# Kernel tuning notes

Measured on AMD Instinct MI355X. Metric: run time of the kernel, lower is better.

The kernel has to match this reference:

```python
import jax, jax.numpy as jnp
import numpy as np

VOCAB = 401
E = 256   # embed_size
H = 768   # hidden_size
O = 3     # output_size
B = 64
T = 1024


def setup_inputs() -> dict:
    key = jax.random.key(0)
    ks = jax.random.split(key, 8)
    s = lambda fan_in: 1.0 / np.sqrt(fan_in)
    return {
        "tokens": jax.random.randint(ks[0], (B, T), 0, VOCAB),
        "hidden": jnp.zeros((B, H), dtype=jnp.float32),
        "embed": jax.random.normal(ks[1], (VOCAB, E), dtype=jnp.float32),
        "W_ih": jax.random.uniform(ks[2], (3 * H, E), jnp.float32, -s(H), s(H)),
        "W_hh": jax.random.uniform(ks[3], (3 * H, H), jnp.float32, -s(H), s(H)),
        "b_ih": jax.random.uniform(ks[4], (3 * H,), jnp.float32, -s(H), s(H)),
        "b_hh": jax.random.uniform(ks[5], (3 * H,), jnp.float32, -s(H), s(H)),
        "W_out": jax.random.uniform(ks[6], (O, H), jnp.float32, -s(H), s(H)),
        "b_out": jax.random.uniform(ks[7], (O,), jnp.float32, -s(H), s(H)),
    }


def reference(tokens, hidden, embed, W_ih, W_hh, b_ih, b_hh, W_out, b_out):
    # Embedding lookup for all timesteps: [B, T, E]
    x = embed[tokens]
    # Precompute input-to-hidden projections for all steps: [B, T, 3H]
    xi = jnp.einsum("bte,ge->btg", x, W_ih) + b_ih
    # Note: original forward zeroes the passed-in hidden; we honor that.
    h0 = jnp.zeros_like(hidden)

    def step(h, xt):  # xt: [B, 3H]
        gh = h @ W_hh.T + b_hh                      # [B, 3H]
        xr, xz, xn = jnp.split(xt, 3, axis=1)
        hr, hz, hn = jnp.split(gh, 3, axis=1)
        r = jax.nn.sigmoid(xr + hr)
        z = jax.nn.sigmoid(xz + hz)
        n = jnp.tanh(xn + r * hn)
        h_new = (1.0 - z) * n + z * h
        return h_new, None

    h_final, _ = jax.lax.scan(step, h0, jnp.swapaxes(xi, 0, 1))  # scan over T
    logits = h_final @ W_out.T + b_out                            # [B, O]
    logprobs = jax.nn.log_softmax(logits, axis=1)
    return (logprobs, h_final)
```

## Files before the change

### kernel.cpp

```cpp
#include <hip/hip_runtime.h>

#define VOCABN 401
#define EN 256
#define HN 768
#define H3N 2304
#define ON 3
#define BN 64
#define TN 1024

#define NREP 16
#define WGPR 16
#define BPR  4
#define JPW  48
#define NTH  768

typedef _Float16 f16x2 __attribute__((ext_vector_type(2)));
typedef _Float16 f16x8 __attribute__((ext_vector_type(8)));
typedef unsigned long long u64;
union F16x8 { f16x8 v; f16x2 p[4]; };

__device__ __forceinline__ float fdot2(f16x2 a, f16x2 b, float c) {
#if __has_builtin(__builtin_amdgcn_fdot2)
    return __builtin_amdgcn_fdot2(a, b, c, false);
#else
    return c + (float)a[0] * (float)b[0] + (float)a[1] * (float)b[1];
#endif
}

__device__ __forceinline__ float hexsum(float x) {
    int v = __builtin_bit_cast(int, x);
    x += __builtin_bit_cast(float, __builtin_amdgcn_update_dpp(0, v, 0xB1, 0xF, 0xF, true));
    v = __builtin_bit_cast(int, x);
    x += __builtin_bit_cast(float, __builtin_amdgcn_update_dpp(0, v, 0x4E, 0xF, 0xF, true));
    v = __builtin_bit_cast(int, x);
    x += __builtin_bit_cast(float, __builtin_amdgcn_update_dpp(0, v, 0x141, 0xF, 0xF, true));
    v = __builtin_bit_cast(int, x);
    x += __builtin_bit_cast(float, __builtin_amdgcn_update_dpp(0, v, 0x140, 0xF, 0xF, true));
    return x;
}

__global__ __launch_bounds__(256)
void k_build_gtab(const float* __restrict__ embed, const float* __restrict__ wih,
                  const float* __restrict__ bih, float* __restrict__ gtab) {
    const int g  = blockIdx.x * 64 + (threadIdx.x >> 2);
    const int ql = threadIdx.x & 3;
    const int v0 = blockIdx.y * 26;
    const int v1 = min(VOCABN, v0 + 26);
    float4 w[16];
    const float4* s4 = (const float4*)(wih + (size_t)g * EN + ql * 64);
#pragma unroll
    for (int i = 0; i < 16; ++i) w[i] = s4[i];
    const float bias = bih[g];
    for (int v = v0; v < v1; ++v) {
        const float4* e4 = (const float4*)(embed + (size_t)v * EN + ql * 64);
        float acc = 0.f;
#pragma unroll
        for (int i = 0; i < 16; ++i) {
            float4 e = e4[i];
            acc += w[i].x * e.x + w[i].y * e.y + w[i].z * e.z + w[i].w * e.w;
        }
        acc += __shfl_xor(acc, 1, 64);
        acc += __shfl_xor(acc, 2, 64);
        if (ql == 0) gtab[(size_t)v * H3N + g] = acc + bias;
    }
}

__global__ __launch_bounds__(NTH, 1)
void k_rnn(const int* __restrict__ tokens, const float* __restrict__ whh,
           const float* __restrict__ gtab, const float* __restrict__ bhh,
           unsigned* __restrict__ hbuf, float* __restrict__ hout) {
    const int R   = blockIdx.x & (NREP - 1);
    const int wg  = blockIdx.x >> 4;
    const int tid = threadIdx.x;
    const int jl  = tid >> 4;
    const int q   = tid & 15;
    const int j   = wg * JPW + jl;

    __shared__ __align__(16) _Float16 hlds[BPR * 16 * 56];
    __shared__ float s_s[3][BPR][JPW];

    F16x8 w[3][6];
#pragma unroll
    for (int g = 0; g < 3; ++g) {
        const float4* s4 = (const float4*)(whh + (size_t)(g * HN + j) * HN + q * 48);
#pragma unroll
        for (int c = 0; c < 6; ++c) {
            float4 a = s4[2 * c], b4 = s4[2 * c + 1];
            F16x8 t;
            t.v[0] = (_Float16)a.x;  t.v[1] = (_Float16)a.y;
            t.v[2] = (_Float16)a.z;  t.v[3] = (_Float16)a.w;
            t.v[4] = (_Float16)b4.x; t.v[5] = (_Float16)b4.y;
            t.v[6] = (_Float16)b4.z; t.v[7] = (_Float16)b4.w;
            w[g][c] = t;
        }
    }

    u64* hb2 = (u64*)hbuf + (size_t)R * (2 * BPR * 384);
    unsigned short* dep = (unsigned short*)hlds + (tid / 24) * 56 + (tid % 24) * 2;

    const int bown  = tid / 48;
    const int jlown = tid - bown * 48;
    const int jown  = wg * JPW + jlown;
    float hprev = 0.f, xr = 0.f, xz = 0.f, xn = 0.f, bhr = 0.f, bhz = 0.f, bhn = 0.f;
    if (tid < 192) {
        bhr = bhh[jown]; bhz = bhh[HN + jown]; bhn = bhh[2 * HN + jown];
        const int tok = tokens[(size_t)(R * BPR + bown) * TN + 0];
        const float* g_ = gtab + (size_t)tok * H3N;
        xr = g_[jown]; xz = g_[HN + jown]; xn = g_[2 * HN + jown];
    }

    u64 vcur = 0, vnxt = 0;
    if (tid < 384) {
        vcur = __hip_atomic_load(hb2 + 0 * 384 + tid, __ATOMIC_RELAXED, __HIP_MEMORY_SCOPE_AGENT);
        vnxt = __hip_atomic_load(hb2 + 1 * 384 + tid, __ATOMIC_RELAXED, __HIP_MEMORY_SCOPE_AGENT);
    }

#pragma unroll 1
    for (int t = 0; t < TN; ++t) {
        const u64 want_pair = ((u64)(unsigned)t << 16) | ((u64)(unsigned)t << 48);
#pragma unroll
        for (int b = 0; b < BPR; ++b) {
            if (tid < 384) {
                const u64* cur = hb2 + ((t & 1) * BPR + b) * 384 + tid;
                while ((vcur & 0xFFFF0000FFFF0000ull) != want_pair) {
                    __builtin_amdgcn_s_sleep(1);
                    vcur = __hip_atomic_load(cur, __ATOMIC_RELAXED, __HIP_MEMORY_SCOPE_AGENT);
                }
                *(unsigned*)(dep + b * 896) =
                    __builtin_amdgcn_perm((unsigned)(vcur >> 32), (unsigned)vcur, 0x05040100);
            }
            __syncthreads();

            if (tid < 384) {
                int b2 = b + 2;
                const int t2 = t + (b2 >> 2);
                b2 &= 3;
                u64 vnew = 0;
                if (t2 < TN)
                    vnew = __hip_atomic_load(hb2 + ((t2 & 1) * BPR + b2) * 384 + tid,
                                             __ATOMIC_RELAXED, __HIP_MEMORY_SCOPE_AGENT);
                vcur = vnxt;
                vnxt = vnew;
            }

            {
                float ar = 0.f, az = 0.f, an = 0.f;
                const f16x8* hp = (const f16x8*)(hlds + b * 896 + q * 56);
#pragma unroll
                for (int c = 0; c < 6; ++c) {
                    F16x8 hh; hh.v = hp[c];
#pragma unroll
                    for (int p = 0; p < 4; ++p) {
                        ar = fdot2(w[0][c].p[p], hh.p[p], ar);
                        az = fdot2(w[1][c].p[p], hh.p[p], az);
                        an = fdot2(w[2][c].p[p], hh.p[p], an);
                    }
                }
                ar = hexsum(ar); az = hexsum(az); an = hexsum(an);
                if (q == 0) {
                    s_s[0][b][jl] = ar; s_s[1][b][jl] = az; s_s[2][b][jl] = an;
                }
            }
            __syncthreads();

            if ((unsigned)(tid - b * 48) < 48u) {
                const float sr = s_s[0][b][jlown];
                const float sz = s_s[1][b][jlown];
                const float sn = s_s[2][b][jlown];
                const float r  = 1.f / (1.f + __expf(-(xr + sr + bhr)));
                const float z  = 1.f / (1.f + __expf(-(xz + sz + bhz)));
                const float nx = xn + r * (sn + bhn);
                const float n  = 1.f - 2.f / (__expf(2.f * nx) + 1.f);
                hprev = (1.f - z) * n + z * hprev;
                unsigned pk = ((unsigned)(t + 1) << 16)
                    | (unsigned)__builtin_bit_cast(unsigned short, (_Float16)hprev);
                const unsigned pk2 = __shfl_down(pk, 1, 64);
                if (t < TN - 1) {
                    if (!(jlown & 1))
                        __hip_atomic_store(
                            hb2 + (((t + 1) & 1) * BPR + b) * 384 + wg * 24 + (jlown >> 1),
                            (u64)pk | ((u64)pk2 << 32),
                            __ATOMIC_RELAXED, __HIP_MEMORY_SCOPE_AGENT);
                    const int tok = tokens[(size_t)(R * BPR + bown) * TN + (t + 1)];
                    const float* g_ = gtab + (size_t)tok * H3N;
                    xr = g_[jown]; xz = g_[HN + jown]; xn = g_[2 * HN + jown];
                } else {
                    hout[(size_t)(R * BPR + bown) * HN + jown] = hprev;
                }
            }
        }
    }
}

__global__ void k_logits(const float* __restrict__ hfin, const float* __restrict__ wout,
                         const float* __restrict__ bout, float* __restrict__ lp) {
    const int b = blockIdx.x;
    const int o = threadIdx.x / 64;
    const int lane = threadIdx.x % 64;
    const float* hrow = hfin + (size_t)b * HN;
    const float* w = wout + (size_t)o * HN;
    float p = 0.f;
    for (int k = lane; k < HN; k += 64) p += hrow[k] * w[k];
    for (int off = 32; off > 0; off >>= 1) p += __shfl_down(p, off, 64);
    __shared__ float lg[ON];
    if (lane == 0) lg[o] = p + bout[o];
    __syncthreads();
    if (threadIdx.x == 0) {
        float m = fmaxf(lg[0], fmaxf(lg[1], lg[2]));
        float s = __expf(lg[0] - m) + __expf(lg[1] - m) + __expf(lg[2] - m);
        float ls = __logf(s);
        lp[b * ON + 0] = lg[0] - m - ls;
        lp[b * ON + 1] = lg[1] - m - ls;
        lp[b * ON + 2] = lg[2] - m - ls;
    }
}

extern "C" void kernel_launch(void* const* d_in, const int* in_sizes, int n_in,
                              void* d_out, int out_size, void* d_ws, size_t ws_size,
                              hipStream_t stream) {
    const int*   tokens = (const int*)d_in[0];
    const float* embed  = (const float*)d_in[2];
    const float* wih    = (const float*)d_in[3];
    const float* whh    = (const float*)d_in[4];
    const float* bih    = (const float*)d_in[5];
    const float* bhh    = (const float*)d_in[6];
    const float* wout   = (const float*)d_in[7];
    const float* bout   = (const float*)d_in[8];

    float* out = (float*)d_out;
    char* ws = (char*)d_ws;
    const size_t GTAB_OFF = 0;
    const size_t HBUF_OFF = 3695616;
    float*    gtab = (float*)(ws + GTAB_OFF);
    unsigned* hbuf = (unsigned*)(ws + HBUF_OFF);

    hipMemsetAsync(ws + HBUF_OFF, 0, 393216, stream);

    hipLaunchKernelGGL(k_build_gtab, dim3(H3N / 64, 16), dim3(256), 0, stream,
                       embed, wih, bih, gtab);
    hipLaunchKernelGGL(k_rnn, dim3(NREP * WGPR), dim3(NTH), 0, stream,
                       tokens, whh, gtab, bhh, hbuf, out + BN * ON);
    hipLaunchKernelGGL(k_logits, dim3(BN), dim3(192), 0, stream,
                       out + BN * ON, wout, bout, out);
}
```

Measured before the change: 5.522 ms.

## Use MFMA 16x16x32 f16 for recurrent matvec with k-split partial sums

Replaces the per-thread fdot2 dot products and DPP hexsum reductions with MFMA 16x16x32 f16 instructions. The weight tile is laid out as MFMA A operands split across 12 waves (3 row groups by 4 k-chunks), and the four k partial sums are combined through LDS. The hidden-state prefetch depth drops from two batches ahead to one, and the barriers become an inline-asm lgkmcnt wait followed by s_barrier. The gate-owner threads move to the last three waves. The MFMA only has one useful output column (a matrix-vector product), so most of its throughput is wasted. The extra LDS partial-sum reduction and the shallower prefetch add latency on the serial critical path.

```diff
diff --git a/kernel.cpp b/kernel.cpp
--- a/kernel.cpp
+++ b/kernel.cpp
@@ -14,29 +14,12 @@
 #define JPW  48
 #define NTH  768
 
-typedef _Float16 f16x2 __attribute__((ext_vector_type(2)));
 typedef _Float16 f16x8 __attribute__((ext_vector_type(8)));
+typedef float f32x4 __attribute__((ext_vector_type(4)));
 typedef unsigned long long u64;
-union F16x8 { f16x8 v; f16x2 p[4]; };
-
-__device__ __forceinline__ float fdot2(f16x2 a, f16x2 b, float c) {
-#if __has_builtin(__builtin_amdgcn_fdot2)
-    return __builtin_amdgcn_fdot2(a, b, c, false);
-#else
-    return c + (float)a[0] * (float)b[0] + (float)a[1] * (float)b[1];
-#endif
-}
-
-__device__ __forceinline__ float hexsum(float x) {
-    int v = __builtin_bit_cast(int, x);
-    x += __builtin_bit_cast(float, __builtin_amdgcn_update_dpp(0, v, 0xB1, 0xF, 0xF, true));
-    v = __builtin_bit_cast(int, x);
-    x += __builtin_bit_cast(float, __builtin_amdgcn_update_dpp(0, v, 0x4E, 0xF, 0xF, true));
-    v = __builtin_bit_cast(int, x);
-    x += __builtin_bit_cast(float, __builtin_amdgcn_update_dpp(0, v, 0x141, 0xF, 0xF, true));
-    v = __builtin_bit_cast(int, x);
-    x += __builtin_bit_cast(float, __builtin_amdgcn_update_dpp(0, v, 0x140, 0xF, 0xF, true));
-    return x;
+
+__device__ __forceinline__ void barrier_lgkm() {
+    asm volatile("s_waitcnt lgkmcnt(0)\n\ts_barrier" ::: "memory");
 }
 
 __global__ __launch_bounds__(256)
@@ -69,51 +52,56 @@
 void k_rnn(const int* __restrict__ tokens, const float* __restrict__ whh,
            const float* __restrict__ gtab, const float* __restrict__ bhh,
            unsigned* __restrict__ hbuf, float* __restrict__ hout) {
-    const int R   = blockIdx.x & (NREP - 1);
-    const int wg  = blockIdx.x >> 4;
-    const int tid = threadIdx.x;
-    const int jl  = tid >> 4;
-    const int q   = tid & 15;
-    const int j   = wg * JPW + jl;
-
-    __shared__ __align__(16) _Float16 hlds[BPR * 16 * 56];
-    __shared__ float s_s[3][BPR][JPW];
-
-    F16x8 w[3][6];
-#pragma unroll
-    for (int g = 0; g < 3; ++g) {
-        const float4* s4 = (const float4*)(whh + (size_t)(g * HN + j) * HN + q * 48);
-#pragma unroll
-        for (int c = 0; c < 6; ++c) {
-            float4 a = s4[2 * c], b4 = s4[2 * c + 1];
-            F16x8 t;
-            t.v[0] = (_Float16)a.x;  t.v[1] = (_Float16)a.y;
-            t.v[2] = (_Float16)a.z;  t.v[3] = (_Float16)a.w;
-            t.v[4] = (_Float16)b4.x; t.v[5] = (_Float16)b4.y;
-            t.v[6] = (_Float16)b4.z; t.v[7] = (_Float16)b4.w;
-            w[g][c] = t;
+    const int R    = blockIdx.x & (NREP - 1);
+    const int wg   = blockIdx.x >> 4;
+    const int tid  = threadIdx.x;
+    const int lane = tid & 63;
+    const int wave = tid >> 6;
+    const int wr   = wave % 3;
+    const int wk   = wave / 3;
+    const int koff8 = ((lane >> 4) & 3) * 8;
+    const int kbase = wk * 192;
+
+    __shared__ __align__(16) _Float16 hT[BPR * HN];
+    __shared__ __align__(16) float psum[4][144];
+
+    f16x8 a[3][6];
+#pragma unroll
+    for (int tt = 0; tt < 3; ++tt) {
+        const int lr  = wr * 48 + tt * 16 + (lane & 15);
+        const int g   = lr / 48;
+        const int jlr = lr % 48;
+        const float* wsrc = whh + (size_t)(g * HN + wg * JPW + jlr) * HN;
+#pragma unroll
+        for (int ks = 0; ks < 6; ++ks) {
+            const float4* p4 = (const float4*)(wsrc + kbase + ks * 32 + koff8);
+            float4 x0 = p4[0], x1 = p4[1];
+            f16x8 t;
+            t[0] = (_Float16)x0.x; t[1] = (_Float16)x0.y;
+            t[2] = (_Float16)x0.z; t[3] = (_Float16)x0.w;
+            t[4] = (_Float16)x1.x; t[5] = (_Float16)x1.y;
+            t[6] = (_Float16)x1.z; t[7] = (_Float16)x1.w;
+            a[tt][ks] = t;
         }
     }
 
     u64* hb2 = (u64*)hbuf + (size_t)R * (2 * BPR * 384);
-    unsigned short* dep = (unsigned short*)hlds + (tid / 24) * 56 + (tid % 24) * 2;
-
-    const int bown  = tid / 48;
-    const int jlown = tid - bown * 48;
+
+    const int gt    = tid - 576;
+    const int bown  = (gt >= 0) ? gt / 48 : 0;
+    const int jlown = (gt >= 0) ? gt - bown * 48 : 0;
     const int jown  = wg * JPW + jlown;
     float hprev = 0.f, xr = 0.f, xz = 0.f, xn = 0.f, bhr = 0.f, bhz = 0.f, bhn = 0.f;
-    if (tid < 192) {
+    if (gt >= 0) {
         bhr = bhh[jown]; bhz = bhh[HN + jown]; bhn = bhh[2 * HN + jown];
         const int tok = tokens[(size_t)(R * BPR + bown) * TN + 0];
         const float* g_ = gtab + (size_t)tok * H3N;
         xr = g_[jown]; xz = g_[HN + jown]; xn = g_[2 * HN + jown];
     }
 
-    u64 vcur = 0, vnxt = 0;
-    if (tid < 384) {
-        vcur = __hip_atomic_load(hb2 + 0 * 384 + tid, __ATOMIC_RELAXED, __HIP_MEMORY_SCOPE_AGENT);
-        vnxt = __hip_atomic_load(hb2 + 1 * 384 + tid, __ATOMIC_RELAXED, __HIP_MEMORY_SCOPE_AGENT);
-    }
+    u64 vin = 0;
+    if (tid < 384)
+        vin = __hip_atomic_load(hb2 + tid, __ATOMIC_RELAXED, __HIP_MEMORY_SCOPE_AGENT);
 
 #pragma unroll 1
     for (int t = 0; t < TN; ++t) {
@@ -122,51 +110,48 @@
         for (int b = 0; b < BPR; ++b) {
             if (tid < 384) {
                 const u64* cur = hb2 + ((t & 1) * BPR + b) * 384 + tid;
-                while ((vcur & 0xFFFF0000FFFF0000ull) != want_pair) {
+                while ((vin & 0xFFFF0000FFFF0000ull) != want_pair) {
                     __builtin_amdgcn_s_sleep(1);
-                    vcur = __hip_atomic_load(cur, __ATOMIC_RELAXED, __HIP_MEMORY_SCOPE_AGENT);
-                }
-                *(unsigned*)(dep + b * 896) =
-                    __builtin_amdgcn_perm((unsigned)(vcur >> 32), (unsigned)vcur, 0x05040100);
+                    vin = __hip_atomic_load(cur, __ATOMIC_RELAXED, __HIP_MEMORY_SCOPE_AGENT);
+                }
+                ((unsigned*)hT)[b * 384 + tid] =
+                    __builtin_amdgcn_perm((unsigned)(vin >> 32), (unsigned)vin, 0x05040100);
+                int b1 = b + 1;
+                const int t1 = t + (b1 >> 2);
+                b1 &= 3;
+                if (t1 < TN)
+                    vin = __hip_atomic_load(hb2 + ((t1 & 1) * BPR + b1) * 384 + tid,
+                                            __ATOMIC_RELAXED, __HIP_MEMORY_SCOPE_AGENT);
             }
-            __syncthreads();
-
-            if (tid < 384) {
-                int b2 = b + 2;
-                const int t2 = t + (b2 >> 2);
-                b2 &= 3;
-                u64 vnew = 0;
-                if (t2 < TN)
-                    vnew = __hip_atomic_load(hb2 + ((t2 & 1) * BPR + b2) * 384 + tid,
-                                             __ATOMIC_RELAXED, __HIP_MEMORY_SCOPE_AGENT);
-                vcur = vnxt;
-                vnxt = vnew;
+            barrier_lgkm();
+
+            {
+                f32x4 acc0 = {0.f, 0.f, 0.f, 0.f};
+                f32x4 acc1 = {0.f, 0.f, 0.f, 0.f};
+                f32x4 acc2 = {0.f, 0.f, 0.f, 0.f};
+#pragma unroll
+                for (int ks = 0; ks < 6; ++ks) {
+                    f16x8 bf = *(const f16x8*)(hT + b * HN + kbase + ks * 32 + koff8);
+                    acc0 = __builtin_amdgcn_mfma_f32_16x16x32_f16(a[0][ks], bf, acc0, 0, 0, 0);
+                    acc1 = __builtin_amdgcn_mfma_f32_16x16x32_f16(a[1][ks], bf, acc1, 0, 0, 0);
+                    acc2 = __builtin_amdgcn_mfma_f32_16x16x32_f16(a[2][ks], bf, acc2, 0, 0, 0);
+                }
+                if ((lane & 15) == 0) {
+                    const int r0 = wr * 48 + ((lane >> 4) & 3) * 4;
+                    *(f32x4*)&psum[wk][r0]      = acc0;
+                    *(f32x4*)&psum[wk][r0 + 16] = acc1;
+                    *(f32x4*)&psum[wk][r0 + 32] = acc2;
+                }
             }
-
-            {
-                float ar = 0.f, az = 0.f, an = 0.f;
-                const f16x8* hp = (const f16x8*)(hlds + b * 896 + q * 56);
-#pragma unroll
-                for (int c = 0; c < 6; ++c) {
-                    F16x8 hh; hh.v = hp[c];
-#pragma unroll
-                    for (int p = 0; p < 4; ++p) {
-                        ar = fdot2(w[0][c].p[p], hh.p[p], ar);
-                        az = fdot2(w[1][c].p[p], hh.p[p], az);
-                        an = fdot2(w[2][c].p[p], hh.p[p], an);
-                    }
-                }
-                ar = hexsum(ar); az = hexsum(az); an = hexsum(an);
-                if (q == 0) {
-                    s_s[0][b][jl] = ar; s_s[1][b][jl] = az; s_s[2][b][jl] = an;
-                }
-            }
-            __syncthreads();
-
-            if ((unsigned)(tid - b * 48) < 48u) {
-                const float sr = s_s[0][b][jlown];
-                const float sz = s_s[1][b][jlown];
-                const float sn = s_s[2][b][jlown];
+            barrier_lgkm();
+
+            if (gt >= 0 && bown == b) {
+                const float sr = (psum[0][jlown]      + psum[1][jlown])
+                               + (psum[2][jlown]      + psum[3][jlown]);
+                const float sz = (psum[0][48 + jlown] + psum[1][48 + jlown])
+                               + (psum[2][48 + jlown] + psum[3][48 + jlown]);
+                const float sn = (psum[0][96 + jlown] + psum[1][96 + jlown])
+                               + (psum[2][96 + jlown] + psum[3][96 + jlown]);
                 const float r  = 1.f / (1.f + __expf(-(xr + sr + bhr)));
                 const float z  = 1.f / (1.f + __expf(-(xz + sz + bhz)));
                 const float nx = xn + r * (sn + bhn);
```

New measurement: 5.506 ms. About the same (-0.3%).
